# Optimization experiments

Measured on AMD Instinct MI355X. Metric: run time of the kernel, lower is better.

## Reference

```python
import jax, jax.numpy as jnp
import numpy as np

B, T, C = 128, 384, 256
H, KV, D = 4, 2, 64          # n_head, n_kv_head, head_dim
REP = H // KV                # query heads per kv head
BLOCK_SIZE = 384


def setup_inputs() -> dict:
    key = jax.random.key(0)
    k0, k1, k2, k3, k4 = jax.random.split(key, 5)
    scale = 0.02
    return {
        "x":  jax.random.normal(k0, (B, T, C), jnp.float32),
        "Wq": jax.random.normal(k1, (C, H * D), jnp.float32) * scale,
        "Wk": jax.random.normal(k2, (C, KV * D), jnp.float32) * scale,
        "Wv": jax.random.normal(k3, (C, KV * D), jnp.float32) * scale,
        "Wo": jax.random.normal(k4, (C, C), jnp.float32) * scale,
    }


def _rope_tables(t_len):
    inv_freq = 1.0 / (10000.0 ** (jnp.arange(0, D, 2, dtype=jnp.float32) / D))
    t = jnp.arange(t_len, dtype=jnp.float32)
    freqs = jnp.outer(t, inv_freq)            # [T, D/2]
    emb = jnp.concatenate([freqs, freqs], -1)  # [T, D]
    return jnp.cos(emb), jnp.sin(emb)


def _rotate_half(x):
    h = x.shape[-1] // 2
    return jnp.concatenate([-x[..., h:], x[..., :h]], -1)


def _apply_rope(x, cos, sin):
    # x: [B, heads, T, D]; cos/sin: [T, D]
    return x * cos[None, None] + _rotate_half(x) * sin[None, None]


def reference(x, Wq, Wk, Wv, Wo):
    b, t, c = x.shape
    q = (x @ Wq).reshape(b, t, H, D).transpose(0, 2, 1, 3)   # [B,H,T,D]
    k = (x @ Wk).reshape(b, t, KV, D).transpose(0, 2, 1, 3)  # [B,KV,T,D]
    v = (x @ Wv).reshape(b, t, KV, D).transpose(0, 2, 1, 3)

    cos, sin = _rope_tables(t)
    q = _apply_rope(q, cos, sin)
    k = _apply_rope(k, cos, sin)

    # GQA: group query heads by kv head instead of repeat_interleave on K/V.
    qg = q.reshape(b, KV, REP, t, D)
    scores = jnp.einsum('bgrtd,bgsd->bgrts', qg, k) / jnp.sqrt(jnp.float32(D))
    causal = jnp.tril(jnp.ones((t, t), dtype=bool))
    scores = jnp.where(causal, scores, jnp.finfo(scores.dtype).min)
    p = jax.nn.softmax(scores, axis=-1)
    y = jnp.einsum('bgrts,bgsd->bgrtd', p, v)                 # [B,KV,REP,T,D]
    y = y.reshape(b, H, t, D).transpose(0, 2, 1, 3).reshape(b, t, c)
    return y @ Wo
```

## Files before the change

### kernel.cpp

```cpp
#include <hip/hip_runtime.h>
#include <hip/hip_bf16.h>

#define BB 128
#define TT 384
#define CC 256
#define HH 4
#define KVH 2
#define QKVW 512
#define MROWS (BB * TT)

#define CVT_BLOCKS 6144

typedef __attribute__((ext_vector_type(8))) short short8;
typedef __attribute__((ext_vector_type(4))) float float4v;

__device__ __forceinline__ unsigned short f2b(float f) {
    union { float f; unsigned u; } v; v.f = f;
    unsigned u = v.u;
    unsigned r = (u + 0x7fffu + ((u >> 16) & 1u)) >> 16;
    return (unsigned short)r;
}
__device__ __forceinline__ float4v mfma16(short8 a, short8 b, float4v c) {
    return __builtin_amdgcn_mfma_f32_16x16x32_bf16(a, b, c, 0, 0, 0);
}
__device__ __forceinline__ void g2lds16(const void* g, void* l) {
    __builtin_amdgcn_global_load_lds(
        (const __attribute__((address_space(1))) unsigned int*)g,
        (__attribute__((address_space(3))) unsigned int*)l, 16, 0, 0);
}
__device__ __forceinline__ unsigned pk2bf(float a, float b) {
    union { float f; unsigned u; } x, y; x.f = a; y.f = b;
    return __builtin_amdgcn_perm(y.u + 0x8000u, x.u + 0x8000u, 0x07060302u);
}

__global__ void prep_kernel(const float* __restrict__ x, unsigned short* __restrict__ xb,
                            const float* __restrict__ Wq, const float* __restrict__ Wk,
                            const float* __restrict__ Wv, const float* __restrict__ Wo,
                            unsigned short* __restrict__ WqkvT, unsigned short* __restrict__ WoT,
                            float* __restrict__ cosT, float* __restrict__ sinT) {
    if (blockIdx.x < CVT_BLOCKS) {
        size_t e = ((size_t)blockIdx.x * 256 + threadIdx.x) * 8;
        const float4* p = (const float4*)(x + e);
        float4 v0 = p[0], v1 = p[1];
        short8 w;
        w[0]=(short)f2b(v0.x); w[1]=(short)f2b(v0.y); w[2]=(short)f2b(v0.z); w[3]=(short)f2b(v0.w);
        w[4]=(short)f2b(v1.x); w[5]=(short)f2b(v1.y); w[6]=(short)f2b(v1.z); w[7]=(short)f2b(v1.w);
        *(short8*)(xb + e) = w;
        return;
    }
    int idx = (blockIdx.x - CVT_BLOCKS) * 256 + threadIdx.x;
    const int N1 = QKVW * CC;
    const int N2 = N1 + CC * CC;
    const int N3 = N2 + TT * 32;
    if (idx < N1) {
        int n = idx >> 8, k = idx & 255;
        float w;
        if (n < 256)      w = Wq[k * 256 + n];
        else if (n < 384) w = Wk[k * 128 + (n - 256)];
        else              w = Wv[k * 128 + (n - 384)];
        WqkvT[n * 256 + k] = f2b(w);
    } else if (idx < N2) {
        int i = idx - N1; int n = i >> 8, k = i & 255;
        WoT[n * 256 + k] = f2b(Wo[k * 256 + n]);
    } else if (idx < N3) {
        int i = idx - N2;
        int t = i >> 5, f = i & 31;
        double invf = exp2(-(double)f / 32.0 * 13.287712379549449);
        double ang = (double)t * invf;
        cosT[t * 32 + f] = (float)cos(ang);
        sinT[t * 32 + f] = (float)sin(ang);
    }
}

__global__ __launch_bounds__(256) void gemm_qkv_kernel(
    const unsigned short* __restrict__ A, const unsigned short* __restrict__ BT,
    unsigned short* __restrict__ Qr, unsigned short* __restrict__ Kr,
    unsigned short* __restrict__ Vt,
    const float* __restrict__ cosT, const float* __restrict__ sinT)
{
    __shared__ __align__(16) unsigned short As[128 * 32];
    __shared__ __align__(16) unsigned short Bs[128 * 32];
    const int tid  = threadIdx.x;
    const int lane = tid & 63;
    const int quad = lane >> 4, l16 = lane & 15;
    const int wave = tid >> 6;
    const int mt = ((blockIdx.x >> 5) << 3) | (blockIdx.x & 7);
    const int nt = (blockIdx.x >> 3) & 3;
    const int mbase = mt * 128, nbase = nt * 128;
    const int wmb = (wave >> 1) * 64, wnb = (wave & 1) * 64;

    float4v acc[4][4] = {};
    const int r0 = tid >> 2, kc = (tid & 3) * 8;
    const int ldsW = (tid & ~63) * 16;
    const unsigned short* gA0 = A  + (size_t)(mbase + r0) * CC + kc;
    const unsigned short* gB0 = BT + (size_t)(nbase + r0) * CC + kc;

    for (int kt = 0; kt < CC; kt += 32) {
        __syncthreads();
        g2lds16(gA0 + kt,                  (char*)As + ldsW);
        g2lds16(gA0 + kt + (size_t)64*CC,  (char*)As + 4096 + ldsW);
        g2lds16(gB0 + kt,                  (char*)Bs + ldsW);
        g2lds16(gB0 + kt + (size_t)64*CC,  (char*)Bs + 4096 + ldsW);
        __syncthreads();

        short8 af[4], bf_[4];
        #pragma unroll
        for (int i = 0; i < 4; i++)
            af[i] = *(const short8*)&As[(wmb + i * 16 + l16) * 32 + quad * 8];
        #pragma unroll
        for (int i = 0; i < 4; i++)
            bf_[i] = *(const short8*)&Bs[(wnb + i * 16 + l16) * 32 + quad * 8];
        #pragma unroll
        for (int i = 0; i < 4; i++)
            #pragma unroll
            for (int j = 0; j < 4; j++)
                acc[i][j] = mfma16(af[i], bf_[j], acc[i][j]);
    }

    const int gn0 = nbase + wnb;
    const int gm0 = mbase + wmb;
    if (gn0 < 384) {
        const bool isq = (gn0 < 256);
        const int  hh  = isq ? (gn0 >> 6) : ((gn0 - 256) >> 6);
        const float qs = isq ? 0.18033688011112042f : 1.0f;
        #pragma unroll
        for (int i = 0; i < 4; i++) {
            #pragma unroll
            for (int r = 0; r < 4; r++) {
                int gm = gm0 + i * 16 + quad * 4 + r;
                int b = gm / TT, t = gm - b * TT;
                unsigned short* dst = isq
                    ? (Qr + (((size_t)b * HH  + hh) * TT + t) * 64)
                    : (Kr + (((size_t)b * KVH + hh) * TT + t) * 64);
                #pragma unroll
                for (int j = 0; j < 2; j++) {
                    int f = j * 16 + l16;
                    float cs = cosT[t * 32 + f], sn = sinT[t * 32 + f];
                    float a  = acc[i][j][r],     c2 = acc[i][j + 2][r];
                    dst[f]      = f2b((a * cs - c2 * sn) * qs);
                    dst[f + 32] = f2b((c2 * cs + a * sn) * qs);
                }
            }
        }
    } else {
        const int g = (gn0 - 384) >> 6;
        #pragma unroll
        for (int i = 0; i < 4; i++) {
            #pragma unroll
            for (int r = 0; r < 4; r++) {
                int gm = gm0 + i * 16 + quad * 4 + r;
                int b = gm / TT, s = gm - b * TT;
                int s6 = s & 63;
                int sig = (s6 & 15) * 4 + (s6 >> 4);
                unsigned short* dst = Vt + (((size_t)b * KVH + g) * 6 + (s >> 6)) * 4096 + sig;
                #pragma unroll
                for (int j = 0; j < 4; j++)
                    dst[(j * 16 + l16) * 64] = f2b(acc[i][j][r]);
            }
        }
    }
}

__global__ __launch_bounds__(256) void gemm_out_kernel(
    const unsigned short* __restrict__ A, const unsigned short* __restrict__ BT,
    float* __restrict__ C)
{
    __shared__ __align__(16) unsigned short As[128 * 32];
    __shared__ __align__(16) unsigned short Bs[128 * 32];
    const int tid  = threadIdx.x;
    const int lane = tid & 63;
    const int quad = lane >> 4, l16 = lane & 15;
    const int wave = tid >> 6;
    const int mt = ((blockIdx.x >> 4) << 3) | (blockIdx.x & 7);
    const int nt = (blockIdx.x >> 3) & 1;
    const int mbase = mt * 128, nbase = nt * 128;
    const int wmb = (wave >> 1) * 64, wnb = (wave & 1) * 64;

    float4v acc[4][4] = {};
    const int r0 = tid >> 2, kc = (tid & 3) * 8;
    const int ldsW = (tid & ~63) * 16;
    const unsigned short* gA0 = A  + (size_t)(mbase + r0) * CC + kc;
    const unsigned short* gB0 = BT + (size_t)(nbase + r0) * CC + kc;

    for (int kt = 0; kt < CC; kt += 32) {
        __syncthreads();
        g2lds16(gA0 + kt,                  (char*)As + ldsW);
        g2lds16(gA0 + kt + (size_t)64*CC,  (char*)As + 4096 + ldsW);
        g2lds16(gB0 + kt,                  (char*)Bs + ldsW);
        g2lds16(gB0 + kt + (size_t)64*CC,  (char*)Bs + 4096 + ldsW);
        __syncthreads();

        short8 af[4], bf_[4];
        #pragma unroll
        for (int i = 0; i < 4; i++)
            af[i] = *(const short8*)&As[(wmb + i * 16 + l16) * 32 + quad * 8];
        #pragma unroll
        for (int i = 0; i < 4; i++)
            bf_[i] = *(const short8*)&Bs[(wnb + i * 16 + l16) * 32 + quad * 8];
        #pragma unroll
        for (int i = 0; i < 4; i++)
            #pragma unroll
            for (int j = 0; j < 4; j++)
                acc[i][j] = mfma16(af[i], bf_[j], acc[i][j]);
    }
    #pragma unroll
    for (int i = 0; i < 4; i++)
        #pragma unroll
        for (int j = 0; j < 4; j++)
            #pragma unroll
            for (int r = 0; r < 4; r++)
                C[(size_t)(mbase + wmb + i * 16 + quad * 4 + r) * CC + nbase + wnb + j * 16 + l16]
                    = acc[i][j][r];
}

__global__ __launch_bounds__(256, 3) void attn_kernel(
    const unsigned short* __restrict__ Qr, const unsigned short* __restrict__ Kr,
    const unsigned short* __restrict__ Vt, unsigned short* __restrict__ y)
{
    __shared__ __align__(16) unsigned short Ks[2][64 * 64];
    __shared__ __align__(16) unsigned short Vs[2][64 * 64];
    __shared__ __align__(16) unsigned short Ps[4][32 * 64];

    const int tid  = threadIdx.x;
    const int lane = tid & 63;
    const int wave = tid >> 6;
    const int quad = lane >> 4, l16 = lane & 15;

    const int xc  = blockIdx.x & 7;
    const int jj  = blockIdx.x >> 3;
    const int p   = jj % 3;
    const int bg  = (jj / 3) * 8 + xc;
    const int g   = bg & 1, b = bg >> 1;
    const int h   = g * 2 + (wave >> 1);

    const unsigned short* Kbase = Kr + ((size_t)b * KVH + g) * TT * 64;
    const unsigned short* Vbase = Vt + ((size_t)b * KVH + g) * 6 * 4096;
    const unsigned short* Qbase = Qr + ((size_t)b * HH + h) * TT * 64;
    unsigned short* ybase = y + (size_t)b * TT * CC + h * 64;
    char* Pw = (char*)&Ps[wave][0];
    const int ldsWave = (tid & ~63) * 16;
    int gc0, gc1;
    { int L0 = tid;       gc0 = ((L0 & ~7) | ((L0 & 7) ^ ((L0 >> 3) & 7))) * 8;
      int L1 = 256 + tid; gc1 = ((L1 & ~7) | ((L1 & 7) ^ ((L1 >> 3) & 7))) * 8; }

    auto stage = [&](int bi, int kt) {
        const unsigned short* kB = Kbase + (size_t)kt * 4096;
        const unsigned short* vB = Vbase + (size_t)kt * 4096;
        g2lds16(kB + gc0, (char*)&Ks[bi][0] + ldsWave);
        g2lds16(kB + gc1, (char*)&Ks[bi][0] + 4096 + ldsWave);
        g2lds16(vB + gc0, (char*)&Vs[bi][0] + ldsWave);
        g2lds16(vB + gc1, (char*)&Vs[bi][0] + 4096 + ldsWave);
    };

    short8 ones;
    #pragma unroll
    for (int j = 0; j < 8; j++) ones[j] = (short)0x3F80;

    int seq = 0;
    stage(0, 0);

    for (int tph = 0; tph < 2; tph++) {
        const int qt = tph ? (5 - p) : p;
        const int qb = qt * 64 + (wave & 1) * 32;

        short8 qf[2][2];
        #pragma unroll
        for (int mi = 0; mi < 2; mi++)
            #pragma unroll
            for (int half = 0; half < 2; half++)
                qf[mi][half] = *(const short8*)(Qbase
                    + (size_t)(qb + mi * 16 + l16) * 64 + half * 32 + quad * 8);

        float4v acc[2][4] = {};
        float4v accl[2]   = {};

        for (int kt = 0; kt <= qt; kt++) {
            __syncthreads();
            if (kt < qt)        stage((seq + 1) & 1, kt + 1);
            else if (tph == 0)  stage((seq + 1) & 1, 0);
            const unsigned short* Kc = &Ks[seq & 1][0];
            const unsigned short* Vc = &Vs[seq & 1][0];

            float4v s_[2][4];
            #pragma unroll
            for (int js = 0; js < 4; js++) {
                int srow = js * 16 + l16, sw = srow & 7;
                short8 kb0 = *(const short8*)((const char*)Kc + srow * 128 + ((quad ^ sw) * 16));
                short8 kb1 = *(const short8*)((const char*)Kc + srow * 128 + (((4 + quad) ^ sw) * 16));
                #pragma unroll
                for (int mi = 0; mi < 2; mi++) {
                    float4v z = {};
                    z = mfma16(qf[mi][0], kb0, z);
                    s_[mi][js] = mfma16(qf[mi][1], kb1, z);
                }
            }

            if (kt == qt) {
                #pragma unroll
                for (int mi = 0; mi < 2; mi++)
                    #pragma unroll
                    for (int js = 0; js < 4; js++) {
                        int coll = js * 16 + l16;
                        #pragma unroll
                        for (int r = 0; r < 4; r++) {
                            int rowl = (wave & 1) * 32 + mi * 16 + quad * 4 + r;
                            if (coll > rowl) s_[mi][js][r] = -1e30f;
                        }
                    }
            }

            #pragma unroll
            for (int mi = 0; mi < 2; mi++)
                #pragma unroll
                for (int r = 0; r < 4; r++) {
                    float e0 = __builtin_amdgcn_exp2f(s_[mi][0][r]);
                    float e1 = __builtin_amdgcn_exp2f(s_[mi][1][r]);
                    float e2 = __builtin_amdgcn_exp2f(s_[mi][2][r]);
                    float e3 = __builtin_amdgcn_exp2f(s_[mi][3][r]);
                    unsigned long long d =
                        (unsigned long long)pk2bf(e0, e1) |
                        ((unsigned long long)pk2bf(e2, e3) << 32);
                    int rho = mi * 16 + quad * 4 + r;
                    int ch  = l16 ^ (((quad * 4 + r) & 7) << 1);
                    *(unsigned long long*)(Pw + rho * 128 + ch * 8) = d;
                }

            short8 pa[2][2];
            #pragma unroll
            for (int mi = 0; mi < 2; mi++)
                #pragma unroll
                for (int half = 0; half < 2; half++) {
                    int chp = (2 * (half * 4 + quad)) ^ ((l16 & 7) << 1);
                    pa[mi][half] = *(const short8*)(Pw + (mi * 16 + l16) * 128 + chp * 8);
                }
            #pragma unroll
            for (int dj = 0; dj < 4; dj++) {
                int vrow = dj * 16 + l16, sw = vrow & 7;
                short8 vb0 = *(const short8*)((const char*)Vc + vrow * 128 + ((quad ^ sw) * 16));
                short8 vb1 = *(const short8*)((const char*)Vc + vrow * 128 + (((4 + quad) ^ sw) * 16));
                #pragma unroll
                for (int mi = 0; mi < 2; mi++) {
                    acc[mi][dj] = mfma16(pa[mi][0], vb0, acc[mi][dj]);
                    acc[mi][dj] = mfma16(pa[mi][1], vb1, acc[mi][dj]);
                }
            }
            #pragma unroll
            for (int mi = 0; mi < 2; mi++) {
                accl[mi] = mfma16(pa[mi][0], ones, accl[mi]);
                accl[mi] = mfma16(pa[mi][1], ones, accl[mi]);
            }
            seq++;
        }

        #pragma unroll
        for (int mi = 0; mi < 2; mi++) {
            float rinv[4];
            #pragma unroll
            for (int r = 0; r < 4; r++) rinv[r] = 1.0f / accl[mi][r];
            #pragma unroll
            for (int dj = 0; dj < 4; dj++)
                #pragma unroll
                for (int r = 0; r < 4; r++) {
                    int tt = qb + mi * 16 + quad * 4 + r;
                    ybase[(size_t)tt * CC + dj * 16 + l16] = f2b(acc[mi][dj][r] * rinv[r]);
                }
        }
    }
}

extern "C" void kernel_launch(void* const* d_in, const int* in_sizes, int n_in,
                              void* d_out, int out_size, void* d_ws, size_t ws_size,
                              hipStream_t stream) {
    const float* x  = (const float*)d_in[0];
    const float* Wq = (const float*)d_in[1];
    const float* Wk = (const float*)d_in[2];
    const float* Wv = (const float*)d_in[3];
    const float* Wo = (const float*)d_in[4];
    float* out = (float*)d_out;

    char* ws = (char*)d_ws;
    size_t off = 0;
    unsigned short* xb = (unsigned short*)(ws + off); off += (size_t)MROWS * CC * 2;
    unsigned short* Qr = (unsigned short*)(ws + off); off += (size_t)BB * HH  * TT * 64 * 2;
    unsigned short* Kr = (unsigned short*)(ws + off); off += (size_t)BB * KVH * TT * 64 * 2;
    unsigned short* Vt = (unsigned short*)(ws + off); off += (size_t)BB * KVH * TT * 64 * 2;
    unsigned short* y  = (unsigned short*)(ws + off); off += (size_t)MROWS * CC * 2;
    unsigned short* WqkvT = (unsigned short*)(ws + off); off += (size_t)QKVW * CC * 2;
    unsigned short* WoT   = (unsigned short*)(ws + off); off += (size_t)CC * CC * 2;
    float* cosT = (float*)(ws + off); off += (size_t)TT * 32 * 4;
    float* sinT = (float*)(ws + off); off += (size_t)TT * 32 * 4;

    prep_kernel<<<CVT_BLOCKS + 816, 256, 0, stream>>>(x, xb, Wq, Wk, Wv, Wo,
                                                      WqkvT, WoT, cosT, sinT);
    gemm_qkv_kernel<<<(MROWS / 128) * 4, 256, 0, stream>>>(xb, WqkvT, Qr, Kr, Vt, cosT, sinT);
    attn_kernel<<<BB * KVH * 3, 256, 0, stream>>>(Qr, Kr, Vt, y);
    gemm_out_kernel<<<(MROWS / 128) * 2, 256, 0, stream>>>(y, WoT, out);
}
```

Measured before the change: 160.7 us.

## Fuse x fp32-to-bf16 conversion into QKV GEMM and double-buffer GEMM LDS tiles

Drops the separate pass that converts x to bf16. The QKV GEMM now loads fp32 x tiles straight into LDS and packs them to bf16 while building MFMA fragments. Both GEMMs switch to double-buffered LDS with one barrier per k-step, so the next tile's loads overlap the current MFMAs, and they request 3 blocks per CU. This removes a full read and write of the activation tensor but doubles the A-tile bytes read per QKV block (each x tile is read by 4 N-tile blocks) and adds LDS pressure from the larger fp32 tiles.

```diff
diff --git a/kernel.cpp b/kernel.cpp
--- a/kernel.cpp
+++ b/kernel.cpp
@@ -9,8 +9,6 @@
 #define QKVW 512
 #define MROWS (BB * TT)
 
-#define CVT_BLOCKS 6144
-
 typedef __attribute__((ext_vector_type(8))) short short8;
 typedef __attribute__((ext_vector_type(4))) float float4v;
 
@@ -33,22 +31,11 @@
     return __builtin_amdgcn_perm(y.u + 0x8000u, x.u + 0x8000u, 0x07060302u);
 }
 
-__global__ void prep_kernel(const float* __restrict__ x, unsigned short* __restrict__ xb,
-                            const float* __restrict__ Wq, const float* __restrict__ Wk,
+__global__ void prep_kernel(const float* __restrict__ Wq, const float* __restrict__ Wk,
                             const float* __restrict__ Wv, const float* __restrict__ Wo,
                             unsigned short* __restrict__ WqkvT, unsigned short* __restrict__ WoT,
                             float* __restrict__ cosT, float* __restrict__ sinT) {
-    if (blockIdx.x < CVT_BLOCKS) {
-        size_t e = ((size_t)blockIdx.x * 256 + threadIdx.x) * 8;
-        const float4* p = (const float4*)(x + e);
-        float4 v0 = p[0], v1 = p[1];
-        short8 w;
-        w[0]=(short)f2b(v0.x); w[1]=(short)f2b(v0.y); w[2]=(short)f2b(v0.z); w[3]=(short)f2b(v0.w);
-        w[4]=(short)f2b(v1.x); w[5]=(short)f2b(v1.y); w[6]=(short)f2b(v1.z); w[7]=(short)f2b(v1.w);
-        *(short8*)(xb + e) = w;
-        return;
-    }
-    int idx = (blockIdx.x - CVT_BLOCKS) * 256 + threadIdx.x;
+    int idx = blockIdx.x * 256 + threadIdx.x;
     const int N1 = QKVW * CC;
     const int N2 = N1 + CC * CC;
     const int N3 = N2 + TT * 32;
@@ -72,14 +59,14 @@
     }
 }
 
-__global__ __launch_bounds__(256) void gemm_qkv_kernel(
-    const unsigned short* __restrict__ A, const unsigned short* __restrict__ BT,
+__global__ __launch_bounds__(256, 3) void gemm_qkv_kernel(
+    const float* __restrict__ A, const unsigned short* __restrict__ BT,
     unsigned short* __restrict__ Qr, unsigned short* __restrict__ Kr,
     unsigned short* __restrict__ Vt,
     const float* __restrict__ cosT, const float* __restrict__ sinT)
 {
-    __shared__ __align__(16) unsigned short As[128 * 32];
-    __shared__ __align__(16) unsigned short Bs[128 * 32];
+    __shared__ __align__(16) float          As[2][128 * 32];
+    __shared__ __align__(16) unsigned short Bs[2][128 * 32];
     const int tid  = threadIdx.x;
     const int lane = tid & 63;
     const int quad = lane >> 4, l16 = lane & 15;
@@ -90,26 +77,41 @@
     const int wmb = (wave >> 1) * 64, wnb = (wave & 1) * 64;
 
     float4v acc[4][4] = {};
-    const int r0 = tid >> 2, kc = (tid & 3) * 8;
     const int ldsW = (tid & ~63) * 16;
-    const unsigned short* gA0 = A  + (size_t)(mbase + r0) * CC + kc;
-    const unsigned short* gB0 = BT + (size_t)(nbase + r0) * CC + kc;
-
-    for (int kt = 0; kt < CC; kt += 32) {
+    const int r0a = tid >> 3, c4 = (tid & 7) * 4;
+    const int r0b = tid >> 2, c8 = (tid & 3) * 8;
+    const float*          gA = A  + (size_t)(mbase + r0a) * CC + c4;
+    const unsigned short* gB = BT + (size_t)(nbase + r0b) * CC + c8;
+
+    auto stage = [&](int bi, int kt) {
+        #pragma unroll
+        for (int i = 0; i < 4; i++)
+            g2lds16(gA + (size_t)i * 32 * CC + kt, (char*)&As[bi][0] + i * 4096 + ldsW);
+        #pragma unroll
+        for (int i = 0; i < 2; i++)
+            g2lds16(gB + (size_t)i * 64 * CC + kt, (char*)&Bs[bi][0] + i * 4096 + ldsW);
+    };
+
+    stage(0, 0);
+    for (int it = 0; it < 8; it++) {
         __syncthreads();
-        g2lds16(gA0 + kt,                  (char*)As + ldsW);
-        g2lds16(gA0 + kt + (size_t)64*CC,  (char*)As + 4096 + ldsW);
-        g2lds16(gB0 + kt,                  (char*)Bs + ldsW);
-        g2lds16(gB0 + kt + (size_t)64*CC,  (char*)Bs + 4096 + ldsW);
-        __syncthreads();
+        if (it < 7) stage((it + 1) & 1, (it + 1) * 32);
+        const int bi = it & 1;
 
         short8 af[4], bf_[4];
         #pragma unroll
-        for (int i = 0; i < 4; i++)
-            af[i] = *(const short8*)&As[(wmb + i * 16 + l16) * 32 + quad * 8];
-        #pragma unroll
-        for (int i = 0; i < 4; i++)
-            bf_[i] = *(const short8*)&Bs[(wnb + i * 16 + l16) * 32 + quad * 8];
+        for (int i = 0; i < 4; i++) {
+            const char* rp = (const char*)&As[bi][0] + (wmb + i * 16 + l16) * 128 + quad * 32;
+            float4 lo = *(const float4*)rp;
+            float4 hi = *(const float4*)(rp + 16);
+            union { short8 s; unsigned u[4]; } t;
+            t.u[0] = pk2bf(lo.x, lo.y); t.u[1] = pk2bf(lo.z, lo.w);
+            t.u[2] = pk2bf(hi.x, hi.y); t.u[3] = pk2bf(hi.z, hi.w);
+            af[i] = t.s;
+        }
+        #pragma unroll
+        for (int i = 0; i < 4; i++)
+            bf_[i] = *(const short8*)&Bs[bi][(wnb + i * 16 + l16) * 32 + quad * 8];
         #pragma unroll
         for (int i = 0; i < 4; i++)
             #pragma unroll
@@ -161,12 +163,12 @@
     }
 }
 
-__global__ __launch_bounds__(256) void gemm_out_kernel(
+__global__ __launch_bounds__(256, 3) void gemm_out_kernel(
     const unsigned short* __restrict__ A, const unsigned short* __restrict__ BT,
     float* __restrict__ C)
 {
-    __shared__ __align__(16) unsigned short As[128 * 32];
-    __shared__ __align__(16) unsigned short Bs[128 * 32];
+    __shared__ __align__(16) unsigned short As[2][128 * 32];
+    __shared__ __align__(16) unsigned short Bs[2][128 * 32];
     const int tid  = threadIdx.x;
     const int lane = tid & 63;
     const int quad = lane >> 4, l16 = lane & 15;
@@ -177,26 +179,31 @@
     const int wmb = (wave >> 1) * 64, wnb = (wave & 1) * 64;
 
     float4v acc[4][4] = {};
+    const int ldsW = (tid & ~63) * 16;
     const int r0 = tid >> 2, kc = (tid & 3) * 8;
-    const int ldsW = (tid & ~63) * 16;
-    const unsigned short* gA0 = A  + (size_t)(mbase + r0) * CC + kc;
-    const unsigned short* gB0 = BT + (size_t)(nbase + r0) * CC + kc;
-
-    for (int kt = 0; kt < CC; kt += 32) {
+    const unsigned short* gA = A  + (size_t)(mbase + r0) * CC + kc;
+    const unsigned short* gB = BT + (size_t)(nbase + r0) * CC + kc;
+
+    auto stage = [&](int bi, int kt) {
+        g2lds16(gA + kt,                  (char*)&As[bi][0] + ldsW);
+        g2lds16(gA + kt + (size_t)64*CC,  (char*)&As[bi][0] + 4096 + ldsW);
+        g2lds16(gB + kt,                  (char*)&Bs[bi][0] + ldsW);
+        g2lds16(gB + kt + (size_t)64*CC,  (char*)&Bs[bi][0] + 4096 + ldsW);
+    };
+
+    stage(0, 0);
+    for (int it = 0; it < 8; it++) {
         __syncthreads();
-        g2lds16(gA0 + kt,                  (char*)As + ldsW);
-        g2lds16(gA0 + kt + (size_t)64*CC,  (char*)As + 4096 + ldsW);
-        g2lds16(gB0 + kt,                  (char*)Bs + ldsW);
-        g2lds16(gB0 + kt + (size_t)64*CC,  (char*)Bs + 4096 + ldsW);
-        __syncthreads();
+        if (it < 7) stage((it + 1) & 1, (it + 1) * 32);
+        const int bi = it & 1;
 
         short8 af[4], bf_[4];
         #pragma unroll
         for (int i = 0; i < 4; i++)
-            af[i] = *(const short8*)&As[(wmb + i * 16 + l16) * 32 + quad * 8];
-        #pragma unroll
-        for (int i = 0; i < 4; i++)
-            bf_[i] = *(const short8*)&Bs[(wnb + i * 16 + l16) * 32 + quad * 8];
+            af[i] = *(const short8*)&As[bi][(wmb + i * 16 + l16) * 32 + quad * 8];
+        #pragma unroll
+        for (int i = 0; i < 4; i++)
+            bf_[i] = *(const short8*)&Bs[bi][(wnb + i * 16 + l16) * 32 + quad * 8];
         #pragma unroll
         for (int i = 0; i < 4; i++)
             #pragma unroll
@@ -380,7 +387,6 @@
 
     char* ws = (char*)d_ws;
     size_t off = 0;
-    unsigned short* xb = (unsigned short*)(ws + off); off += (size_t)MROWS * CC * 2;
     unsigned short* Qr = (unsigned short*)(ws + off); off += (size_t)BB * HH  * TT * 64 * 2;
     unsigned short* Kr = (unsigned short*)(ws + off); off += (size_t)BB * KVH * TT * 64 * 2;
     unsigned short* Vt = (unsigned short*)(ws + off); off += (size_t)BB * KVH * TT * 64 * 2;
@@ -390,9 +396,8 @@
     float* cosT = (float*)(ws + off); off += (size_t)TT * 32 * 4;
     float* sinT = (float*)(ws + off); off += (size_t)TT * 32 * 4;
 
-    prep_kernel<<<CVT_BLOCKS + 816, 256, 0, stream>>>(x, xb, Wq, Wk, Wv, Wo,
-                                                      WqkvT, WoT, cosT, sinT);
-    gemm_qkv_kernel<<<(MROWS / 128) * 4, 256, 0, stream>>>(xb, WqkvT, Qr, Kr, Vt, cosT, sinT);
+    prep_kernel<<<816, 256, 0, stream>>>(Wq, Wk, Wv, Wo, WqkvT, WoT, cosT, sinT);
+    gemm_qkv_kernel<<<(MROWS / 128) * 4, 256, 0, stream>>>(x, WqkvT, Qr, Kr, Vt, cosT, sinT);
     attn_kernel<<<BB * KVH * 3, 256, 0, stream>>>(Qr, Kr, Vt, y);
     gemm_out_kernel<<<(MROWS / 128) * 2, 256, 0, stream>>>(y, WoT, out);
 }
```

Measured after the change: 167.7 us. +4.4%, slower.
